# Kernel tuning notes

Measured on AMD Instinct MI355X. Metric: run time of the kernel, lower is better.

The kernel has to match this reference:

```python
import jax, jax.numpy as jnp
import numpy as np

N = 50000
E = 625000
D_IN = 128
D_OUT = 128
NEG_SLOPE = 0.01  # torch LeakyReLU default


def setup_inputs() -> dict:
    key = jax.random.key(0)
    k1, k2, k3, k4, k5, k6, k7, k8 = jax.random.split(key, 8)
    features = jax.random.normal(k1, (N, D_IN), dtype=jnp.float32)
    target = jax.random.randint(k2, (E,), 0, N, dtype=jnp.int64)
    neighbor = jax.random.randint(k3, (E,), 0, N, dtype=jnp.int64)
    values = jax.random.uniform(k4, (E,), dtype=jnp.float32)
    # nn.Linear params (kaiming-uniform-ish init: U(-1/sqrt(in), 1/sqrt(in)))
    bound = 1.0 / np.sqrt(D_IN)
    W1 = jax.random.uniform(k5, (D_OUT, D_IN), minval=-bound, maxval=bound, dtype=jnp.float32)
    b1 = jax.random.uniform(k6, (D_OUT,), minval=-bound, maxval=bound, dtype=jnp.float32)
    W2 = jax.random.uniform(k7, (D_OUT, D_IN), minval=-bound, maxval=bound, dtype=jnp.float32)
    b2 = jax.random.uniform(k8, (D_OUT,), minval=-bound, maxval=bound, dtype=jnp.float32)
    return {"features": features, "target": target, "neighbor": neighbor,
            "values": values, "W1": W1, "b1": b1, "W2": W2, "b2": b2}


def reference(features, target, neighbor, values, W1, b1, W2, b2):
    # gather-scale: msg[e] = features[neighbor[e]] * values[e]
    msg = features[neighbor] * values[:, None]              # (E, D_IN)
    # scatter-add into target nodes
    h_neigh = jax.ops.segment_sum(msg, target, num_segments=N)  # (N, D_IN)
    # dual linear fusion + leaky relu
    h = (features + h_neigh) @ W1.T + b1 + (features * h_neigh) @ W2.T + b2
    return jnp.where(h >= 0, h, NEG_SLOPE * h)
```

## Files before the change

### kernel.cpp

```cpp
#include <hip/hip_runtime.h>

#define D 128
#define CAP 40
#define NEG_SLOPE 0.01f

typedef float v4f __attribute__((ext_vector_type(4)));
typedef short short8 __attribute__((ext_vector_type(8)));

static __device__ __forceinline__ short f2bf(float f) {
    unsigned u = __float_as_uint(f);
    unsigned r = (u + 0x7fffu + ((u >> 16) & 1u)) >> 16;
    return (short)r;
}
static __device__ __forceinline__ float bflo(unsigned u) { return __uint_as_float(u << 16); }
static __device__ __forceinline__ float bfhi(unsigned u) { return __uint_as_float(u & 0xffff0000u); }
static __device__ __forceinline__ unsigned packbf(float x, float y) {
    return (unsigned)(unsigned short)f2bf(x) | ((unsigned)(unsigned short)f2bf(y) << 16);
}

__global__ __launch_bounds__(256) void conv_kernel(const float* __restrict__ feat,
                                                   const float* __restrict__ W1,
                                                   const float* __restrict__ W2,
                                                   unsigned* __restrict__ featbf,
                                                   short* __restrict__ Wbf,
                                                   int* __restrict__ deg,
                                                   int nPairs, int nNodes) {
    int i = blockIdx.x * 256 + threadIdx.x;
    if (i < nPairs) {
        float2 f = ((const float2*)feat)[i];
        featbf[i] = packbf(f.x, f.y);
    }
    if (i < D * D) {
        Wbf[i]         = f2bf(W1[i]);
        Wbf[D * D + i] = f2bf(W2[i]);
    }
    if (i < nNodes) deg[i] = 0;
}

__global__ __launch_bounds__(256) void bucket_kernel(const int* __restrict__ tgt,
                                                     const int* __restrict__ nbr,
                                                     const float* __restrict__ vals,
                                                     int* __restrict__ deg,
                                                     int2* __restrict__ edata, int E) {
    int e = blockIdx.x * 256 + threadIdx.x;
    if (e >= E) return;
    int t    = tgt[e];
    int slot = atomicAdd(&deg[t], 1);
    if (slot < CAP) {
        int2 ed;
        ed.x = nbr[e];
        ed.y = __float_as_int(vals[e]);
        edata[(long)t * CAP + slot] = ed;
    }
}

__global__ __launch_bounds__(256) void gather_kernel(const unsigned* __restrict__ featbf,
                                                     const int2* __restrict__ edata,
                                                     const int* __restrict__ deg,
                                                     const int* __restrict__ tgt,
                                                     const int* __restrict__ nbr,
                                                     const float* __restrict__ vals,
                                                     unsigned* __restrict__ X1,
                                                     unsigned* __restrict__ X2,
                                                     int nNodes, int E) {
    int wid  = (blockIdx.x * 256 + threadIdx.x) >> 6;
    int lane = threadIdx.x & 63;
    if (wid >= nNodes) return;
    int d = deg[wid];

    unsigned uf = featbf[(long)wid * (D / 2) + lane];

    float ax0 = 0.f, ay0 = 0.f, ax1 = 0.f, ay1 = 0.f;
    float ax2 = 0.f, ay2 = 0.f, ax3 = 0.f, ay3 = 0.f;

    if (d <= CAP) {
        const int4* ep4 = (const int4*)(edata + (long)wid * CAP);
        int j = 0;
        for (; j + 8 <= d; j += 8) {
            int4 p0 = ep4[(j >> 1) + 0];
            int4 p1 = ep4[(j >> 1) + 1];
            int4 p2 = ep4[(j >> 1) + 2];
            int4 p3 = ep4[(j >> 1) + 3];
            unsigned u0 = featbf[(long)p0.x * (D / 2) + lane];
            unsigned u1 = featbf[(long)p0.z * (D / 2) + lane];
            unsigned u2 = featbf[(long)p1.x * (D / 2) + lane];
            unsigned u3 = featbf[(long)p1.z * (D / 2) + lane];
            unsigned u4 = featbf[(long)p2.x * (D / 2) + lane];
            unsigned u5 = featbf[(long)p2.z * (D / 2) + lane];
            unsigned u6 = featbf[(long)p3.x * (D / 2) + lane];
            unsigned u7 = featbf[(long)p3.z * (D / 2) + lane];
            float v0 = __int_as_float(p0.y), v1 = __int_as_float(p0.w);
            float v2 = __int_as_float(p1.y), v3 = __int_as_float(p1.w);
            float v4 = __int_as_float(p2.y), v5 = __int_as_float(p2.w);
            float v6 = __int_as_float(p3.y), v7 = __int_as_float(p3.w);
            ax0 += bflo(u0) * v0; ay0 += bfhi(u0) * v0;
            ax1 += bflo(u1) * v1; ay1 += bfhi(u1) * v1;
            ax2 += bflo(u2) * v2; ay2 += bfhi(u2) * v2;
            ax3 += bflo(u3) * v3; ay3 += bfhi(u3) * v3;
            ax0 += bflo(u4) * v4; ay0 += bfhi(u4) * v4;
            ax1 += bflo(u5) * v5; ay1 += bfhi(u5) * v5;
            ax2 += bflo(u6) * v6; ay2 += bfhi(u6) * v6;
            ax3 += bflo(u7) * v7; ay3 += bfhi(u7) * v7;
        }
        for (; j + 2 <= d; j += 2) {
            int4 p = ep4[j >> 1];
            unsigned u0 = featbf[(long)p.x * (D / 2) + lane];
            unsigned u1 = featbf[(long)p.z * (D / 2) + lane];
            float v0 = __int_as_float(p.y), v1 = __int_as_float(p.w);
            ax0 += bflo(u0) * v0; ay0 += bfhi(u0) * v0;
            ax1 += bflo(u1) * v1; ay1 += bfhi(u1) * v1;
        }
        if (j < d) {
            int2 p = edata[(long)wid * CAP + j];
            unsigned u = featbf[(long)p.x * (D / 2) + lane];
            float v = __int_as_float(p.y);
            ax0 += bflo(u) * v; ay0 += bfhi(u) * v;
        }
    } else {
        for (int base = 0; base < E; base += 64) {
            int e = base + lane;
            int t = (e < E) ? tgt[e] : -1;
            unsigned long long m = __ballot(t == wid);
            while (m) {
                int b = __ffsll((long long)m) - 1;
                m &= m - 1;
                int   ee = base + b;
                int   nb = nbr[ee];
                float v  = vals[ee];
                unsigned u = featbf[(long)nb * (D / 2) + lane];
                ax0 += bflo(u) * v;
                ay0 += bfhi(u) * v;
            }
        }
    }

    float accx = (ax0 + ax1) + (ax2 + ax3);
    float accy = (ay0 + ay1) + (ay2 + ay3);
    float fx = bflo(uf), fy = bfhi(uf);
    X1[(long)wid * (D / 2) + lane] = packbf(fx + accx, fy + accy);
    X2[(long)wid * (D / 2) + lane] = packbf(fx * accx, fy * accy);
}

__global__ __launch_bounds__(256) void gemm_kernel(const short* __restrict__ X1s,
                                                   const short* __restrict__ X2s,
                                                   const short* __restrict__ Wbf,
                                                   const float* __restrict__ b1,
                                                   const float* __restrict__ b2,
                                                   float* __restrict__ out, int nNodes) {
    __shared__ __align__(16) short sW[2 * D * D];

    int tid = threadIdx.x;
    for (int c = tid; c < 4096; c += 256) {
        int r  = c >> 4;
        int cc = c & 15;
        int pp = cc ^ (r & 15);
        *(short8*)(&sW[r * D + pp * 8]) = *(const short8*)(Wbf + c * 8);
    }
    __syncthreads();

    int lane = tid & 63;
    int wid  = (blockIdx.x * 256 + tid) >> 6;
    int m0   = wid * 32;
    if (m0 >= nNodes) return;
    bool t2 = (m0 + 16) < nNodes;

    int mrow = lane & 15;
    int quad = lane >> 4;

    const short* xa1 = X1s + (long)(m0 + mrow) * D + quad * 8;
    const short* xa2 = X2s + (long)(m0 + mrow) * D + quad * 8;
    const short* xb1 = xa1 + 16 * D;
    const short* xb2 = xa2 + 16 * D;

    v4f acc[2][8];
#pragma unroll
    for (int t = 0; t < 2; t++)
#pragma unroll
        for (int i = 0; i < 8; i++) acc[t][i] = (v4f)(0.0f);

#pragma unroll
    for (int s = 0; s < 4; s++) {
        short8 a1 = *(const short8*)(xa1 + s * 32);
        short8 a2 = *(const short8*)(xa2 + s * 32);
        short8 c1, c2;
        if (t2) {
            c1 = *(const short8*)(xb1 + s * 32);
            c2 = *(const short8*)(xb2 + s * 32);
        }
        int pp = (s * 4 + quad) ^ mrow;
#pragma unroll
        for (int ot = 0; ot < 8; ot++) {
            int row = ot * 16 + mrow;
            short8 w1 = *(const short8*)(&sW[row * D + pp * 8]);
            short8 w2 = *(const short8*)(&sW[D * D + row * D + pp * 8]);
            acc[0][ot] = __builtin_amdgcn_mfma_f32_16x16x32_bf16(a1, w1, acc[0][ot], 0, 0, 0);
            acc[0][ot] = __builtin_amdgcn_mfma_f32_16x16x32_bf16(a2, w2, acc[0][ot], 0, 0, 0);
            if (t2) {
                acc[1][ot] = __builtin_amdgcn_mfma_f32_16x16x32_bf16(c1, w1, acc[1][ot], 0, 0, 0);
                acc[1][ot] = __builtin_amdgcn_mfma_f32_16x16x32_bf16(c2, w2, acc[1][ot], 0, 0, 0);
            }
        }
    }

#pragma unroll
    for (int ot = 0; ot < 8; ot++) {
        int   o    = ot * 16 + mrow;
        float bias = b1[o] + b2[o];
#pragma unroll
        for (int r = 0; r < 4; r++) {
            int   node = m0 + quad * 4 + r;
            float v    = acc[0][ot][r] + bias;
            out[(long)node * D + o] = (v >= 0.0f) ? v : NEG_SLOPE * v;
            if (t2) {
                float w = acc[1][ot][r] + bias;
                out[(long)(node + 16) * D + o] = (w >= 0.0f) ? w : NEG_SLOPE * w;
            }
        }
    }
}

extern "C" void kernel_launch(void* const* d_in, const int* in_sizes, int n_in,
                              void* d_out, int out_size, void* d_ws, size_t ws_size,
                              hipStream_t stream) {
    const float* feat = (const float*)d_in[0];
    const int*   tgt  = (const int*)d_in[1];
    const int*   nbr  = (const int*)d_in[2];
    const float* vals = (const float*)d_in[3];
    const float* W1   = (const float*)d_in[4];
    const float* b1   = (const float*)d_in[5];
    const float* W2   = (const float*)d_in[6];
    const float* b2   = (const float*)d_in[7];
    float*       out  = (float*)d_out;

    int E      = in_sizes[1];
    int nNodes = out_size / D;

    int*      deg    = (int*)d_ws;
    int2*     edata  = (int2*)(deg + nNodes);
    short*    Wbf    = (short*)(edata + (long)nNodes * CAP);
    unsigned* featbf = (unsigned*)(Wbf + 2 * D * D);
    unsigned* X1     = featbf + (long)nNodes * (D / 2);
    unsigned* X2     = X1 + (long)nNodes * (D / 2);

    int nPairs = nNodes * (D / 2);

    conv_kernel<<<(nPairs + 255) / 256, 256, 0, stream>>>(feat, W1, W2, featbf, Wbf, deg, nPairs, nNodes);
    bucket_kernel<<<(E + 255) / 256, 256, 0, stream>>>(tgt, nbr, vals, deg, edata, E);
    gather_kernel<<<(nNodes * 64 + 255) / 256, 256, 0, stream>>>(featbf, edata, deg, tgt, nbr, vals,
                                                                 X1, X2, nNodes, E);

    int nPairTiles = (nNodes + 31) / 32;
    int nBlocks    = (nPairTiles + 3) / 4;
    gemm_kernel<<<nBlocks, 256, 0, stream>>>((const short*)X1, (const short*)X2, Wbf, b1, b2, out, nNodes);
}
```

Measured before the change: 175.4 us.

## Fuse conversion with bucketing, branchless gather loop, larger GEMM blocks

Merges the bf16 conversion kernel and the edge bucketing kernel into one launch and zeroes degrees with a memset instead. Replaces the gather's unrolled, pairwise and tail loops with a single 8-wide loop that clamps indices and zeroes weights for padding edges. Doubles GEMM block size to 512 threads so each block's shared-memory weight load serves twice as many tiles, and hoists the bias loads before the main loop. The gather now does wasted loads on padded slots, and the fused kernel relies on nPairs being at least E so every edge is covered.

```diff
diff --git a/kernel.cpp b/kernel.cpp
--- a/kernel.cpp
+++ b/kernel.cpp
@@ -18,13 +18,17 @@
     return (unsigned)(unsigned short)f2bf(x) | ((unsigned)(unsigned short)f2bf(y) << 16);
 }
 
-__global__ __launch_bounds__(256) void conv_kernel(const float* __restrict__ feat,
-                                                   const float* __restrict__ W1,
-                                                   const float* __restrict__ W2,
-                                                   unsigned* __restrict__ featbf,
-                                                   short* __restrict__ Wbf,
-                                                   int* __restrict__ deg,
-                                                   int nPairs, int nNodes) {
+__global__ __launch_bounds__(256) void convbucket_kernel(const float* __restrict__ feat,
+                                                         const float* __restrict__ W1,
+                                                         const float* __restrict__ W2,
+                                                         const int* __restrict__ tgt,
+                                                         const int* __restrict__ nbr,
+                                                         const float* __restrict__ vals,
+                                                         unsigned* __restrict__ featbf,
+                                                         short* __restrict__ Wbf,
+                                                         int* __restrict__ deg,
+                                                         int2* __restrict__ edata,
+                                                         int nPairs, int E) {
     int i = blockIdx.x * 256 + threadIdx.x;
     if (i < nPairs) {
         float2 f = ((const float2*)feat)[i];
@@ -34,23 +38,15 @@
         Wbf[i]         = f2bf(W1[i]);
         Wbf[D * D + i] = f2bf(W2[i]);
     }
-    if (i < nNodes) deg[i] = 0;
-}
-
-__global__ __launch_bounds__(256) void bucket_kernel(const int* __restrict__ tgt,
-                                                     const int* __restrict__ nbr,
-                                                     const float* __restrict__ vals,
-                                                     int* __restrict__ deg,
-                                                     int2* __restrict__ edata, int E) {
-    int e = blockIdx.x * 256 + threadIdx.x;
-    if (e >= E) return;
-    int t    = tgt[e];
-    int slot = atomicAdd(&deg[t], 1);
-    if (slot < CAP) {
-        int2 ed;
-        ed.x = nbr[e];
-        ed.y = __float_as_int(vals[e]);
-        edata[(long)t * CAP + slot] = ed;
+    if (i < E) {
+        int t    = tgt[i];
+        int slot = atomicAdd(&deg[t], 1);
+        if (slot < CAP) {
+            int2 ed;
+            ed.x = nbr[i];
+            ed.y = __float_as_int(vals[i]);
+            edata[(long)t * CAP + slot] = ed;
+        }
     }
 }
 
@@ -74,25 +70,33 @@
     float ax2 = 0.f, ay2 = 0.f, ax3 = 0.f, ay3 = 0.f;
 
     if (d <= CAP) {
-        const int4* ep4 = (const int4*)(edata + (long)wid * CAP);
-        int j = 0;
-        for (; j + 8 <= d; j += 8) {
-            int4 p0 = ep4[(j >> 1) + 0];
-            int4 p1 = ep4[(j >> 1) + 1];
-            int4 p2 = ep4[(j >> 1) + 2];
-            int4 p3 = ep4[(j >> 1) + 3];
+        const int2* ep = edata + (long)wid * CAP;
+        int dm1 = d - 1;
+        for (int j = 0; j < d; j += 8) {
+            int2 p0 = ep[min(j + 0, dm1)];
+            int2 p1 = ep[min(j + 1, dm1)];
+            int2 p2 = ep[min(j + 2, dm1)];
+            int2 p3 = ep[min(j + 3, dm1)];
+            int2 p4 = ep[min(j + 4, dm1)];
+            int2 p5 = ep[min(j + 5, dm1)];
+            int2 p6 = ep[min(j + 6, dm1)];
+            int2 p7 = ep[min(j + 7, dm1)];
             unsigned u0 = featbf[(long)p0.x * (D / 2) + lane];
-            unsigned u1 = featbf[(long)p0.z * (D / 2) + lane];
-            unsigned u2 = featbf[(long)p1.x * (D / 2) + lane];
-            unsigned u3 = featbf[(long)p1.z * (D / 2) + lane];
-            unsigned u4 = featbf[(long)p2.x * (D / 2) + lane];
-            unsigned u5 = featbf[(long)p2.z * (D / 2) + lane];
-            unsigned u6 = featbf[(long)p3.x * (D / 2) + lane];
-            unsigned u7 = featbf[(long)p3.z * (D / 2) + lane];
-            float v0 = __int_as_float(p0.y), v1 = __int_as_float(p0.w);
-            float v2 = __int_as_float(p1.y), v3 = __int_as_float(p1.w);
-            float v4 = __int_as_float(p2.y), v5 = __int_as_float(p2.w);
-            float v6 = __int_as_float(p3.y), v7 = __int_as_float(p3.w);
+            unsigned u1 = featbf[(long)p1.x * (D / 2) + lane];
+            unsigned u2 = featbf[(long)p2.x * (D / 2) + lane];
+            unsigned u3 = featbf[(long)p3.x * (D / 2) + lane];
+            unsigned u4 = featbf[(long)p4.x * (D / 2) + lane];
+            unsigned u5 = featbf[(long)p5.x * (D / 2) + lane];
+            unsigned u6 = featbf[(long)p6.x * (D / 2) + lane];
+            unsigned u7 = featbf[(long)p7.x * (D / 2) + lane];
+            float v0 = (j + 0 < d) ? __int_as_float(p0.y) : 0.0f;
+            float v1 = (j + 1 < d) ? __int_as_float(p1.y) : 0.0f;
+            float v2 = (j + 2 < d) ? __int_as_float(p2.y) : 0.0f;
+            float v3 = (j + 3 < d) ? __int_as_float(p3.y) : 0.0f;
+            float v4 = (j + 4 < d) ? __int_as_float(p4.y) : 0.0f;
+            float v5 = (j + 5 < d) ? __int_as_float(p5.y) : 0.0f;
+            float v6 = (j + 6 < d) ? __int_as_float(p6.y) : 0.0f;
+            float v7 = (j + 7 < d) ? __int_as_float(p7.y) : 0.0f;
             ax0 += bflo(u0) * v0; ay0 += bfhi(u0) * v0;
             ax1 += bflo(u1) * v1; ay1 += bfhi(u1) * v1;
             ax2 += bflo(u2) * v2; ay2 += bfhi(u2) * v2;
@@ -101,20 +105,6 @@
             ax1 += bflo(u5) * v5; ay1 += bfhi(u5) * v5;
             ax2 += bflo(u6) * v6; ay2 += bfhi(u6) * v6;
             ax3 += bflo(u7) * v7; ay3 += bfhi(u7) * v7;
-        }
-        for (; j + 2 <= d; j += 2) {
-            int4 p = ep4[j >> 1];
-            unsigned u0 = featbf[(long)p.x * (D / 2) + lane];
-            unsigned u1 = featbf[(long)p.z * (D / 2) + lane];
-            float v0 = __int_as_float(p.y), v1 = __int_as_float(p.w);
-            ax0 += bflo(u0) * v0; ay0 += bfhi(u0) * v0;
-            ax1 += bflo(u1) * v1; ay1 += bfhi(u1) * v1;
-        }
-        if (j < d) {
-            int2 p = edata[(long)wid * CAP + j];
-            unsigned u = featbf[(long)p.x * (D / 2) + lane];
-            float v = __int_as_float(p.y);
-            ax0 += bflo(u) * v; ay0 += bfhi(u) * v;
         }
     } else {
         for (int base = 0; base < E; base += 64) {
@@ -141,7 +131,7 @@
     X2[(long)wid * (D / 2) + lane] = packbf(fx * accx, fy * accy);
 }
 
-__global__ __launch_bounds__(256) void gemm_kernel(const short* __restrict__ X1s,
+__global__ __launch_bounds__(512) void gemm_kernel(const short* __restrict__ X1s,
                                                    const short* __restrict__ X2s,
                                                    const short* __restrict__ Wbf,
                                                    const float* __restrict__ b1,
@@ -150,7 +140,7 @@
     __shared__ __align__(16) short sW[2 * D * D];
 
     int tid = threadIdx.x;
-    for (int c = tid; c < 4096; c += 256) {
+    for (int c = tid; c < 4096; c += 512) {
         int r  = c >> 4;
         int cc = c & 15;
         int pp = cc ^ (r & 15);
@@ -159,13 +149,20 @@
     __syncthreads();
 
     int lane = tid & 63;
-    int wid  = (blockIdx.x * 256 + tid) >> 6;
+    int wid  = (blockIdx.x * 512 + tid) >> 6;
     int m0   = wid * 32;
     if (m0 >= nNodes) return;
     bool t2 = (m0 + 16) < nNodes;
 
     int mrow = lane & 15;
     int quad = lane >> 4;
+
+    float bias[8];
+#pragma unroll
+    for (int ot = 0; ot < 8; ot++) {
+        int o = ot * 16 + mrow;
+        bias[ot] = b1[o] + b2[o];
+    }
 
     const short* xa1 = X1s + (long)(m0 + mrow) * D + quad * 8;
     const short* xa2 = X2s + (long)(m0 + mrow) * D + quad * 8;
@@ -204,15 +201,14 @@
 
 #pragma unroll
     for (int ot = 0; ot < 8; ot++) {
-        int   o    = ot * 16 + mrow;
-        float bias = b1[o] + b2[o];
+        int o = ot * 16 + mrow;
 #pragma unroll
         for (int r = 0; r < 4; r++) {
             int   node = m0 + quad * 4 + r;
-            float v    = acc[0][ot][r] + bias;
+            float v    = acc[0][ot][r] + bias[ot];
             out[(long)node * D + o] = (v >= 0.0f) ? v : NEG_SLOPE * v;
             if (t2) {
-                float w = acc[1][ot][r] + bias;
+                float w = acc[1][ot][r] + bias[ot];
                 out[(long)(node + 16) * D + o] = (w >= 0.0f) ? w : NEG_SLOPE * w;
             }
         }
@@ -244,12 +240,13 @@
 
     int nPairs = nNodes * (D / 2);
 
-    conv_kernel<<<(nPairs + 255) / 256, 256, 0, stream>>>(feat, W1, W2, featbf, Wbf, deg, nPairs, nNodes);
-    bucket_kernel<<<(E + 255) / 256, 256, 0, stream>>>(tgt, nbr, vals, deg, edata, E);
+    hipMemsetAsync(deg, 0, (size_t)nNodes * sizeof(int), stream);
+    convbucket_kernel<<<(nPairs + 255) / 256, 256, 0, stream>>>(feat, W1, W2, tgt, nbr, vals,
+                                                                featbf, Wbf, deg, edata, nPairs, E);
     gather_kernel<<<(nNodes * 64 + 255) / 256, 256, 0, stream>>>(featbf, edata, deg, tgt, nbr, vals,
                                                                  X1, X2, nNodes, E);
 
     int nPairTiles = (nNodes + 31) / 32;
-    int nBlocks    = (nPairTiles + 3) / 4;
-    gemm_kernel<<<nBlocks, 256, 0, stream>>>((const short*)X1, (const short*)X2, Wbf, b1, b2, out, nNodes);
-}
+    int nBlocks    = (nPairTiles + 7) / 8;
+    gemm_kernel<<<nBlocks, 512, 0, stream>>>((const short*)X1, (const short*)X2, Wbf, b1, b2, out, nNodes);
+}
```

New measurement: 171.9 us. -2.0%, faster.
